# Kernel tuning notes

Measured on AMD Instinct MI355X. Metric: run time of the kernel, lower is better.

Reference implementation:

```python
import jax, jax.numpy as jnp
import numpy as np

N, E = 20000, 5000
IN_FT, OUT_FT = 128, 128
DENSITY = 0.01  # fraction of nonzeros in the incidence matrix


def setup_inputs() -> dict:
    key = jax.random.key(0)
    kx, kh, kw, kb = jax.random.split(key, 4)
    X = jax.random.normal(kx, (N, IN_FT), dtype=jnp.float32)
    H = (jax.random.uniform(kh, (N, E)) < DENSITY).astype(jnp.float32)
    # xavier_normal_ with gain=0.01
    xav_std = 0.01 * np.sqrt(2.0 / (IN_FT + OUT_FT))
    weight_trans = jax.random.normal(kw, (IN_FT, OUT_FT), dtype=jnp.float32) * xav_std
    bias = jax.random.normal(kb, (OUT_FT,), dtype=jnp.float32) * 0.01
    return {"X": X, "H": H, "weight_trans": weight_trans, "bias": bias}


def reference(X, H, weight_trans, bias):
    # X: [N, in_ft], H: [N, E] incidence
    Xw = X @ weight_trans                      # [N, out_ft]
    DV = jnp.sum(H, axis=1) + 1e-12            # node degrees, [N]
    DE = jnp.sum(H, axis=0) + 1e-12            # hyperedge degrees, [E]
    # G = diag(1/DV) @ H @ diag(1/DE) @ H^T applied to Xw, computed in the
    # efficient order without materializing the NxN matrix G:
    M = H.T @ Xw                               # [E, out_ft]
    M = M / DE[:, None]                        # diag(1/DE) scaling
    out = H @ M                                # [N, out_ft]
    out = out / DV[:, None]                    # diag(1/DV) scaling
    out = out + bias
    return jax.nn.relu(out)
```

## Files before the change

### kernel.cpp

```cpp
#include <hip/hip_runtime.h>
#include <hip/hip_bf16.h>

typedef unsigned long long u64;
typedef __attribute__((ext_vector_type(4))) float f32x4v;
typedef __attribute__((ext_vector_type(8))) unsigned short u16x8;

#define N_NODES 20000
#define N_EDGES 5000
#define FT 128
#define NT 20
#define NRG 313
#define ROW_U64 80
#define COL_STRIDE 5120
#define MAX_DEG 320
#define MAX_NDEG 128

#define NTLOAD(p) __builtin_nontemporal_load((const f32x4v*)(p))

__global__ __launch_bounds__(256) void scan_fused(
    const float* __restrict__ H, u64* __restrict__ Hbt, u64* __restrict__ HbtT,
    const float2* __restrict__ X2, __hip_bfloat162* __restrict__ Xb2) {
  const int wid = threadIdx.x >> 6, lane = threadIdx.x & 63;

  if (blockIdx.x >= 1565) {
    for (int i = (blockIdx.x - 1565) * 256 + threadIdx.x; i < 1280000;
         i += 320 * 256)
      Xb2[i] = __float22bfloat162_rn(X2[i]);
    return;
  }

  const int gw = blockIdx.x * 4 + wid;
  const int t = gw % NT, rg = gw / NT;
  const int r0 = rg * 64;
  const int rows = min(64, N_NODES - r0);
  const int idx4 = t * 64 + lane;
  const bool lv = idx4 < 1250;

  u64 m0 = 0, m1 = 0, m2 = 0, m3 = 0;
  for (int kb = 0; kb < rows; kb += 8) {
    f32x4v vv[8];
#pragma unroll
    for (int k = 0; k < 8; ++k) vv[k] = (f32x4v){0.f, 0.f, 0.f, 0.f};
    if (lv) {
      const float* bp = H + (size_t)(r0 + kb) * N_EDGES + idx4 * 4;
#pragma unroll
      for (int k = 0; k < 8; ++k) vv[k] = NTLOAD(bp + (size_t)k * N_EDGES);
    }
#pragma unroll
    for (int k = 0; k < 8; ++k) {
      u64 b0 = __ballot(vv[k].x != 0.f);
      u64 b1 = __ballot(vv[k].y != 0.f);
      u64 b2 = __ballot(vv[k].z != 0.f);
      u64 b3 = __ballot(vv[k].w != 0.f);
      const bool keep = (lane == kb + k);
      m0 = keep ? b0 : m0;  m1 = keep ? b1 : m1;
      m2 = keep ? b2 : m2;  m3 = keep ? b3 : m3;
    }
  }
  if (lane < rows) {
    u64* hp = Hbt + (size_t)(r0 + lane) * ROW_U64 + t * 4;
    hp[0] = m0; hp[1] = m1; hp[2] = m2; hp[3] = m3;
  }
  u64 t0 = 0, t1 = 0, t2 = 0, t3 = 0;
  for (int l = 0; l < 64; ++l) {
    u64 c0 = __ballot((m0 >> l) & 1ull);
    u64 c1 = __ballot((m1 >> l) & 1ull);
    u64 c2 = __ballot((m2 >> l) & 1ull);
    u64 c3 = __ballot((m3 >> l) & 1ull);
    const bool keep = (lane == l);
    t0 = keep ? c0 : t0;  t1 = keep ? c1 : t1;
    t2 = keep ? c2 : t2;  t3 = keep ? c3 : t3;
  }
  u64* op = HbtT + (size_t)rg * COL_STRIDE + t * 256 + 4 * lane;
  op[0] = t0; op[1] = t1; op[2] = t2; op[3] = t3;
}

__global__ __launch_bounds__(256) void edge_gather(
    const u16x8* __restrict__ Xb8,
    const u64* __restrict__ HbtT,
    f32x4v* __restrict__ P4, int* __restrict__ de) {
  __shared__ int sidx[4][MAX_DEG];
  const int wid = threadIdx.x >> 6, lane = threadIdx.x & 63;
  const int e = blockIdx.x * 4 + wid;

  u64 cm[5];
#pragma unroll
  for (int q = 0; q < 5; ++q) {
    int u = q * 64 + lane;
    cm[q] = (u < NRG) ? HbtT[(size_t)u * COL_STRIDE + e] : 0ull;
  }
  int cnt = 0;
#pragma unroll
  for (int q = 0; q < 5; ++q) cnt += __popcll(cm[q]);
  int off = cnt;
  for (int d = 1; d < 64; d <<= 1) {
    int v = __shfl_up(off, d);
    if (lane >= d) off += v;
  }
  int total = __shfl(off, 63);
  off -= cnt;
#pragma unroll
  for (int q = 0; q < 5; ++q) {
    u64 w = cm[q];
    int rbase = q * 4096 + lane * 64;
    while (w) {
      int b = __ffsll(w) - 1;
      w &= w - 1;
      if (off < MAX_DEG) sidx[wid][off] = rbase + b;
      ++off;
    }
  }
  __builtin_amdgcn_s_waitcnt(0);
  int tt = min(total, MAX_DEG);

  const int ug = lane >> 4;
  const int li = lane & 15;
  float acc[8];
#pragma unroll
  for (int j = 0; j < 8; ++j) acc[j] = 0.f;

  int g = 0;
  for (; g + 32 <= tt; g += 32) {
    int nn[8];
#pragma unroll
    for (int q = 0; q < 8; ++q) nn[q] = sidx[wid][g + 4 * q + ug];
    u16x8 vv[8];
#pragma unroll
    for (int q = 0; q < 8; ++q) vv[q] = Xb8[(size_t)nn[q] * 16 + li];
#pragma unroll
    for (int q = 0; q < 8; ++q)
#pragma unroll
      for (int j = 0; j < 8; ++j)
        acc[j] += __uint_as_float((unsigned)vv[q][j] << 16);
  }
  for (; g < tt; g += 4) {
    int r = g + ug;
    bool ok = r < tt;
    int n0 = sidx[wid][ok ? r : g];
    u16x8 vv = Xb8[(size_t)n0 * 16 + li];
    if (ok) {
#pragma unroll
      for (int j = 0; j < 8; ++j)
        acc[j] += __uint_as_float((unsigned)vv[j] << 16);
    }
  }
#pragma unroll
  for (int j = 0; j < 8; ++j) {
    acc[j] += __shfl_xor(acc[j], 16);
    acc[j] += __shfl_xor(acc[j], 32);
  }
  if (lane < 16) {
    f32x4v lo = {acc[0], acc[1], acc[2], acc[3]};
    f32x4v hi = {acc[4], acc[5], acc[6], acc[7]};
    P4[(size_t)e * 32 + 2 * li] = lo;
    P4[(size_t)e * 32 + 2 * li + 1] = hi;
  }
  if (lane == 0) de[e] = total;
}

__global__ __launch_bounds__(256) void gemm_M(
    const float* __restrict__ P, const float* __restrict__ W,
    const int* __restrict__ de, float* __restrict__ M) {
  int f = threadIdx.x & (FT - 1);
  int half = threadIdx.x >> 7;
  int e = blockIdx.x * 8 + half * 4;
  const float* p0 = P + (e + 0) * FT;
  const float* p1 = P + (e + 1) * FT;
  const float* p2 = P + (e + 2) * FT;
  const float* p3 = P + (e + 3) * FT;
  float a0 = 0.f, a1 = 0.f, a2 = 0.f, a3 = 0.f;
#pragma unroll 4
  for (int k = 0; k < FT; ++k) {
    float w = W[k * FT + f];
    a0 += p0[k] * w; a1 += p1[k] * w; a2 += p2[k] * w; a3 += p3[k] * w;
  }
  M[(e + 0) * FT + f] = a0 / ((float)de[e + 0] + 1e-12f);
  M[(e + 1) * FT + f] = a1 / ((float)de[e + 1] + 1e-12f);
  M[(e + 2) * FT + f] = a2 / ((float)de[e + 2] + 1e-12f);
  M[(e + 3) * FT + f] = a3 / ((float)de[e + 3] + 1e-12f);
}

__global__ __launch_bounds__(256) void row_apply(
    const u64* __restrict__ Hbt,
    const f32x4v* __restrict__ M4, const f32x4v* __restrict__ bias4,
    f32x4v* __restrict__ out4) {
  __shared__ int eidx[4][MAX_NDEG];
  const int wid = threadIdx.x >> 6, lane = threadIdx.x & 63;
  const int n = blockIdx.x * 4 + wid;
  const u64* hp = Hbt + (size_t)n * ROW_U64;
  u64 mlo = hp[lane];
  u64 mhi = (lane < ROW_U64 - 64) ? hp[64 + lane] : 0ull;
  int cnt = __popcll(mlo) + __popcll(mhi);
  int off = cnt;
  for (int d = 1; d < 64; d <<= 1) {
    int v = __shfl_up(off, d);
    if (lane >= d) off += v;
  }
  int total = __shfl(off, 63);
  off -= cnt;
  {
    int eb = (lane >> 2) * 256 + (lane & 3);
    u64 w = mlo;
    while (w) {
      int b = __ffsll(w) - 1; w &= w - 1;
      if (off < MAX_NDEG) eidx[wid][off] = eb + 4 * b;
      ++off;
    }
    int vp = 64 + lane;
    eb = (vp >> 2) * 256 + (vp & 3);
    w = mhi;
    while (w) {
      int b = __ffsll(w) - 1; w &= w - 1;
      if (off < MAX_NDEG) eidx[wid][off] = eb + 4 * b;
      ++off;
    }
  }
  __builtin_amdgcn_s_waitcnt(0);
  int tt = min(total, MAX_NDEG);

  const int uh = lane >> 5;
  const int li = lane & 31;
  float a0 = 0.f, a1 = 0.f, a2 = 0.f, a3 = 0.f;
  int g = 0;
  for (; g + 16 <= tt; g += 16) {
    int ee[8];
#pragma unroll
    for (int q = 0; q < 8; ++q) ee[q] = eidx[wid][g + 2 * q + uh];
    f32x4v vv[8];
#pragma unroll
    for (int q = 0; q < 8; ++q) vv[q] = M4[(size_t)ee[q] * 32 + li];
#pragma unroll
    for (int q = 0; q < 8; ++q) {
      a0 += vv[q][0]; a1 += vv[q][1]; a2 += vv[q][2]; a3 += vv[q][3];
    }
  }
  for (; g < tt; g += 2) {
    int r = g + uh;
    bool ok = r < tt;
    int ee = eidx[wid][ok ? r : g];
    f32x4v vv = M4[(size_t)ee * 32 + li];
    if (ok) { a0 += vv[0]; a1 += vv[1]; a2 += vv[2]; a3 += vv[3]; }
  }
  a0 += __shfl_xor(a0, 32);
  a1 += __shfl_xor(a1, 32);
  a2 += __shfl_xor(a2, 32);
  a3 += __shfl_xor(a3, 32);
  if (lane < 32) {
    float inv = 1.f / ((float)total + 1e-12f);
    f32x4v bb = bias4[li];
    f32x4v o;
    o[0] = fmaxf(fmaf(a0, inv, bb[0]), 0.f);
    o[1] = fmaxf(fmaf(a1, inv, bb[1]), 0.f);
    o[2] = fmaxf(fmaf(a2, inv, bb[2]), 0.f);
    o[3] = fmaxf(fmaf(a3, inv, bb[3]), 0.f);
    out4[(size_t)n * 32 + li] = o;
  }
}

extern "C" void kernel_launch(void* const* d_in, const int* in_sizes, int n_in,
                              void* d_out, int out_size, void* d_ws, size_t ws_size,
                              hipStream_t stream) {
  const float* X    = (const float*)d_in[0];
  const float* H    = (const float*)d_in[1];
  const float* W    = (const float*)d_in[2];
  const float* bias = (const float*)d_in[3];
  float* out = (float*)d_out;

  int* ws = (int*)d_ws;
  u64* Hbt             = (u64*)ws;
  u64* HbtT            = (u64*)(ws + 3200000);
  __hip_bfloat162* Xb2 = (__hip_bfloat162*)(ws + 6476800);
  float* P             = (float*)(ws + 7756800);
  int* de              = ws + 8396800;
  float* M             = (float*)(ws + 8401920);

  scan_fused <<<1885, 256, 0, stream>>>(H, Hbt, HbtT, (const float2*)X, Xb2);
  edge_gather<<<1250, 256, 0, stream>>>((const u16x8*)Xb2, HbtT,
                                        (f32x4v*)P, de);
  gemm_M     <<<625, 256, 0, stream>>>(P, W, de, M);
  row_apply  <<<5000, 256, 0, stream>>>(Hbt, (const f32x4v*)M,
                                        (const f32x4v*)bias, (f32x4v*)out);
}
```

Measured before the change: 589.9 us.

## Fuse weight GEMM into edge gather and store M as bf16

Merges the separate gemm_M kernel into the edge gather kernel. The per-edge sums go into shared memory and are multiplied by W in place, removing one launch and the round trip of P and the degree array through global memory. M is now written in bf16, which halves the gather traffic in row_apply; its loop is reworked to 16-lane groups decoding bf16. The cost is lower precision in M and redundant W reads per block.

```diff
diff --git a/kernel.cpp b/kernel.cpp
--- a/kernel.cpp
+++ b/kernel.cpp
@@ -2,6 +2,8 @@
 #include <hip/hip_bf16.h>
 
 typedef unsigned long long u64;
+typedef unsigned int u32;
+typedef unsigned short u16;
 typedef __attribute__((ext_vector_type(4))) float f32x4v;
 typedef __attribute__((ext_vector_type(8))) unsigned short u16x8;
 
@@ -17,6 +19,12 @@
 
 #define NTLOAD(p) __builtin_nontemporal_load((const f32x4v*)(p))
 
+static __device__ __forceinline__ u16 f2bf(float x) {
+  u32 u = __float_as_uint(x);
+  u = (u + 0x7FFFu + ((u >> 16) & 1u)) >> 16;
+  return (u16)u;
+}
+
 __global__ __launch_bounds__(256) void scan_fused(
     const float* __restrict__ H, u64* __restrict__ Hbt, u64* __restrict__ HbtT,
     const float2* __restrict__ X2, __hip_bfloat162* __restrict__ Xb2) {
@@ -75,13 +83,17 @@
   op[0] = t0; op[1] = t1; op[2] = t2; op[3] = t3;
 }
 
-__global__ __launch_bounds__(256) void edge_gather(
+__global__ __launch_bounds__(256) void edge_gather_m(
     const u16x8* __restrict__ Xb8,
     const u64* __restrict__ HbtT,
-    f32x4v* __restrict__ P4, int* __restrict__ de) {
+    const float* __restrict__ W,
+    u16* __restrict__ Mb) {
   __shared__ int sidx[4][MAX_DEG];
+  __shared__ float Pt[4][FT];
+  __shared__ float sde[4];
   const int wid = threadIdx.x >> 6, lane = threadIdx.x & 63;
-  const int e = blockIdx.x * 4 + wid;
+  const int e0 = blockIdx.x * 4;
+  const int e = e0 + wid;
 
   u64 cm[5];
 #pragma unroll
@@ -150,40 +162,30 @@
     acc[j] += __shfl_xor(acc[j], 32);
   }
   if (lane < 16) {
-    f32x4v lo = {acc[0], acc[1], acc[2], acc[3]};
-    f32x4v hi = {acc[4], acc[5], acc[6], acc[7]};
-    P4[(size_t)e * 32 + 2 * li] = lo;
-    P4[(size_t)e * 32 + 2 * li + 1] = hi;
-  }
-  if (lane == 0) de[e] = total;
-}
-
-__global__ __launch_bounds__(256) void gemm_M(
-    const float* __restrict__ P, const float* __restrict__ W,
-    const int* __restrict__ de, float* __restrict__ M) {
-  int f = threadIdx.x & (FT - 1);
-  int half = threadIdx.x >> 7;
-  int e = blockIdx.x * 8 + half * 4;
-  const float* p0 = P + (e + 0) * FT;
-  const float* p1 = P + (e + 1) * FT;
-  const float* p2 = P + (e + 2) * FT;
-  const float* p3 = P + (e + 3) * FT;
-  float a0 = 0.f, a1 = 0.f, a2 = 0.f, a3 = 0.f;
+#pragma unroll
+    for (int j = 0; j < 8; ++j) Pt[wid][8 * lane + j] = acc[j];
+  }
+  if (lane == 0) sde[wid] = (float)total + 1e-12f;
+  __syncthreads();
+
+  {
+    const int f = threadIdx.x & 127, eh = threadIdx.x >> 7;
+    float a0 = 0.f, a1 = 0.f;
 #pragma unroll 4
-  for (int k = 0; k < FT; ++k) {
-    float w = W[k * FT + f];
-    a0 += p0[k] * w; a1 += p1[k] * w; a2 += p2[k] * w; a3 += p3[k] * w;
-  }
-  M[(e + 0) * FT + f] = a0 / ((float)de[e + 0] + 1e-12f);
-  M[(e + 1) * FT + f] = a1 / ((float)de[e + 1] + 1e-12f);
-  M[(e + 2) * FT + f] = a2 / ((float)de[e + 2] + 1e-12f);
-  M[(e + 3) * FT + f] = a3 / ((float)de[e + 3] + 1e-12f);
+    for (int k = 0; k < FT; ++k) {
+      float w = W[k * FT + f];
+      a0 += Pt[eh][k] * w;
+      a1 += Pt[eh + 2][k] * w;
+    }
+    Mb[(size_t)(e0 + eh) * FT + f]     = f2bf(a0 / sde[eh]);
+    Mb[(size_t)(e0 + eh + 2) * FT + f] = f2bf(a1 / sde[eh + 2]);
+  }
 }
 
 __global__ __launch_bounds__(256) void row_apply(
     const u64* __restrict__ Hbt,
-    const f32x4v* __restrict__ M4, const f32x4v* __restrict__ bias4,
-    f32x4v* __restrict__ out4) {
+    const u16x8* __restrict__ Mb8,
+    const f32x4v* __restrict__ bias4, f32x4v* __restrict__ out4) {
   __shared__ int eidx[4][MAX_NDEG];
   const int wid = threadIdx.x >> 6, lane = threadIdx.x & 63;
   const int n = blockIdx.x * 4 + wid;
@@ -218,42 +220,53 @@
   __builtin_amdgcn_s_waitcnt(0);
   int tt = min(total, MAX_NDEG);
 
-  const int uh = lane >> 5;
-  const int li = lane & 31;
-  float a0 = 0.f, a1 = 0.f, a2 = 0.f, a3 = 0.f;
+  const int rq = lane >> 4;
+  const int li = lane & 15;
+  float acc[8];
+#pragma unroll
+  for (int j = 0; j < 8; ++j) acc[j] = 0.f;
+
   int g = 0;
-  for (; g + 16 <= tt; g += 16) {
+  for (; g + 32 <= tt; g += 32) {
     int ee[8];
 #pragma unroll
-    for (int q = 0; q < 8; ++q) ee[q] = eidx[wid][g + 2 * q + uh];
-    f32x4v vv[8];
-#pragma unroll
-    for (int q = 0; q < 8; ++q) vv[q] = M4[(size_t)ee[q] * 32 + li];
-#pragma unroll
-    for (int q = 0; q < 8; ++q) {
-      a0 += vv[q][0]; a1 += vv[q][1]; a2 += vv[q][2]; a3 += vv[q][3];
-    }
-  }
-  for (; g < tt; g += 2) {
-    int r = g + uh;
+    for (int q = 0; q < 8; ++q) ee[q] = eidx[wid][g + 4 * q + rq];
+    u16x8 vv[8];
+#pragma unroll
+    for (int q = 0; q < 8; ++q) vv[q] = Mb8[(size_t)ee[q] * 16 + li];
+#pragma unroll
+    for (int q = 0; q < 8; ++q)
+#pragma unroll
+      for (int j = 0; j < 8; ++j)
+        acc[j] += __uint_as_float((unsigned)vv[q][j] << 16);
+  }
+  for (; g < tt; g += 4) {
+    int r = g + rq;
     bool ok = r < tt;
     int ee = eidx[wid][ok ? r : g];
-    f32x4v vv = M4[(size_t)ee * 32 + li];
-    if (ok) { a0 += vv[0]; a1 += vv[1]; a2 += vv[2]; a3 += vv[3]; }
-  }
-  a0 += __shfl_xor(a0, 32);
-  a1 += __shfl_xor(a1, 32);
-  a2 += __shfl_xor(a2, 32);
-  a3 += __shfl_xor(a3, 32);
-  if (lane < 32) {
+    u16x8 vv = Mb8[(size_t)ee * 16 + li];
+    if (ok) {
+#pragma unroll
+      for (int j = 0; j < 8; ++j)
+        acc[j] += __uint_as_float((unsigned)vv[j] << 16);
+    }
+  }
+#pragma unroll
+  for (int j = 0; j < 8; ++j) {
+    acc[j] += __shfl_xor(acc[j], 16);
+    acc[j] += __shfl_xor(acc[j], 32);
+  }
+  if (lane < 16) {
     float inv = 1.f / ((float)total + 1e-12f);
-    f32x4v bb = bias4[li];
-    f32x4v o;
-    o[0] = fmaxf(fmaf(a0, inv, bb[0]), 0.f);
-    o[1] = fmaxf(fmaf(a1, inv, bb[1]), 0.f);
-    o[2] = fmaxf(fmaf(a2, inv, bb[2]), 0.f);
-    o[3] = fmaxf(fmaf(a3, inv, bb[3]), 0.f);
-    out4[(size_t)n * 32 + li] = o;
+    f32x4v b0 = bias4[2 * lane], b1 = bias4[2 * lane + 1];
+    f32x4v o0, o1;
+#pragma unroll
+    for (int j = 0; j < 4; ++j) {
+      o0[j] = fmaxf(fmaf(acc[j], inv, b0[j]), 0.f);
+      o1[j] = fmaxf(fmaf(acc[4 + j], inv, b1[j]), 0.f);
+    }
+    out4[(size_t)n * 32 + 2 * lane]     = o0;
+    out4[(size_t)n * 32 + 2 * lane + 1] = o1;
   }
 }
 
@@ -270,14 +283,10 @@
   u64* Hbt             = (u64*)ws;
   u64* HbtT            = (u64*)(ws + 3200000);
   __hip_bfloat162* Xb2 = (__hip_bfloat162*)(ws + 6476800);
-  float* P             = (float*)(ws + 7756800);
-  int* de              = ws + 8396800;
-  float* M             = (float*)(ws + 8401920);
-
-  scan_fused <<<1885, 256, 0, stream>>>(H, Hbt, HbtT, (const float2*)X, Xb2);
-  edge_gather<<<1250, 256, 0, stream>>>((const u16x8*)Xb2, HbtT,
-                                        (f32x4v*)P, de);
-  gemm_M     <<<625, 256, 0, stream>>>(P, W, de, M);
-  row_apply  <<<5000, 256, 0, stream>>>(Hbt, (const f32x4v*)M,
-                                        (const f32x4v*)bias, (f32x4v*)out);
-}
+  u16* Mb              = (u16*)(ws + 7756800);
+
+  scan_fused   <<<1885, 256, 0, stream>>>(H, Hbt, HbtT, (const float2*)X, Xb2);
+  edge_gather_m<<<1250, 256, 0, stream>>>((const u16x8*)Xb2, HbtT, W, Mb);
+  row_apply    <<<5000, 256, 0, stream>>>(Hbt, (const u16x8*)Mb,
+                                          (const f32x4v*)bias, (f32x4v*)out);
+}
```

Result: faster. 572.0 us (-3.0%).
